# Performance work log

Hardware: AMD Instinct MI355X
Metric: run time of the kernel (lower is better)

Reference implementation:

```python
import jax, jax.numpy as jnp
from jax import lax
import numpy as np

T, B, NI, D = 512, 128, 512, 512  # time, batch, input dim, hidden dim


def setup_inputs() -> dict:
    key = jax.random.key(0)
    k1, k2, k3, k4 = jax.random.split(key, 4)
    stdv = 1.0 / np.sqrt(D)
    return {
        "X": jax.random.normal(k1, (T, B, NI), dtype=jnp.float32),
        "Wf": jax.random.uniform(k2, (NI, 4 * D), jnp.float32, -stdv, stdv),
        "Wr": jax.random.uniform(k3, (D, 4 * D), jnp.float32, -stdv, stdv),
        "bf": jax.random.uniform(k4, (4 * D,), jnp.float32, -2 * stdv, 2 * stdv),
        "i": jnp.ones((T, B), dtype=jnp.float32),
        "h0": jnp.zeros((B, D), dtype=jnp.float32),
        "c0": jnp.zeros((B, D), dtype=jnp.float32),
    }


def reference(X, Wf, Wr, bf, i, h0, c0):
    # Precompute input contribution to all gates: [T, B, 4D]
    intern = jnp.einsum('tbi,ig->tbg', X, Wf) + bf

    def step(carry, inp):
        h, c = carry           # h: [B,D] (previous masked output), c: [B,D]
        z, m = inp             # z: [B,4D], m: [B] validity mask
        z = z + h @ Wr
        cin = jnp.tanh(z[:, :D])                 # cell input
        ig = jax.nn.sigmoid(z[:, D:2 * D])       # input gate
        fg = jax.nn.sigmoid(z[:, 2 * D:3 * D])   # forget gate
        og = jax.nn.sigmoid(z[:, 3 * D:])        # output gate
        m = m[:, None]
        c_new = m * (c * fg + cin * ig) + (1.0 - m) * c
        y = m * (og * jnp.tanh(c_new))           # output zeroed on invalid frames
        return (y, c_new), (y, c_new)

    (_, d), (Y, C) = lax.scan(step, (h0, c0), (intern, i))
    # Matches module: returns (Y, (C, d)) -> flattened here
    return Y, C, d
```

## Files before the change

kernel.cpp:

```cpp
#include <hip/hip_runtime.h>
#include <hip/hip_bf16.h>
#include <hip/hip_fp16.h>

#define T_STEPS 512
#define BATCH   128
#define NID     512
#define DH      512
#define KTOT    1024
#define NG      2048

using f16x8 = __attribute__((ext_vector_type(8))) _Float16;
using f32x4 = __attribute__((ext_vector_type(4))) float;

__device__ __forceinline__ float sigmoid_fast(float x) {
    return 1.0f / (1.0f + __expf(-x));
}
__device__ __forceinline__ float tanh_fast(float x) {
    float ax = fabsf(x);
    float e = __expf(2.0f * ax);
    float r = 1.0f - 2.0f / (e + 1.0f);
    return copysignf(r, x);
}

__global__ void prep_weights(const float* __restrict__ Wf,
                             const float* __restrict__ Wr,
                             const float* __restrict__ bf,
                             _Float16* __restrict__ WT,
                             float* __restrict__ bfa) {
    int orow = blockIdx.x;
    int d = orow >> 2;
    int g = orow & 3;
    int col = g * DH + d;
    for (int e = 0; e < 4; ++e) {
        int k = (e << 8) + threadIdx.x;
        float v = (k < NID) ? Wf[(size_t)k * NG + col]
                            : Wr[(size_t)(k - NID) * NG + col];
        WT[(size_t)orow * KTOT + k] = (_Float16)v;
    }
    if (threadIdx.x == 0) bfa[orow] = bf[col];
}

__global__ void prep_state(const float* __restrict__ h0,
                           const float* __restrict__ c0,
                           _Float16* __restrict__ h,
                           float* __restrict__ c) {
    int base = blockIdx.x * 1024 + threadIdx.x;
    for (int e = 0; e < 4; ++e) {
        int i = base + e * 256;
        h[i] = (_Float16)h0[i];
        c[i] = c0[i];
    }
}

__global__ __launch_bounds__(256)
void lstm_step(const float* __restrict__ X,
               const float* __restrict__ imask,
               const _Float16* __restrict__ WT,
               const float* __restrict__ bfa,
               const _Float16* __restrict__ hin,
               _Float16* __restrict__ hout,
               float* __restrict__ c,
               float* __restrict__ Yout,
               float* __restrict__ Cout,
               float* __restrict__ dout,
               int t) {
    __shared__ float zs[32][68];

    const int tid  = threadIdx.x;
    const int lane = tid & 63;
    const int w    = tid >> 6;
    const int l15  = lane & 15;
    const int l4   = lane >> 4;

    const int b0  = blockIdx.x * 32;
    const int gc0 = blockIdx.y * 64;

    const int rt  = w & 1;
    const int ct0 = (w >> 1) * 2;

    const int arow = b0 + rt * 16 + l15;
    const float*    xrow = X + ((size_t)t * BATCH + arow) * NID;
    const _Float16* hrow = hin + (size_t)arow * DH;

    const int koff = l4 * 8;

    const _Float16* bp0 = WT + (size_t)(gc0 + 16 * ct0 + l15) * KTOT + koff;
    const _Float16* bp1 = WT + (size_t)(gc0 + 16 * (ct0 + 1) + l15) * KTOT + koff;

    f32x4 acc0 = {0.f, 0.f, 0.f, 0.f};
    f32x4 acc1 = {0.f, 0.f, 0.f, 0.f};

    #pragma unroll 4
    for (int k0 = 0; k0 < KTOT; k0 += 32) {
        f16x8 a;
        if (k0 < NID) {
            const float* xp = xrow + k0 + koff;
            f32x4 v0 = *(const f32x4*)xp;
            f32x4 v1 = *(const f32x4*)(xp + 4);
            a[0] = (_Float16)v0[0]; a[1] = (_Float16)v0[1];
            a[2] = (_Float16)v0[2]; a[3] = (_Float16)v0[3];
            a[4] = (_Float16)v1[0]; a[5] = (_Float16)v1[1];
            a[6] = (_Float16)v1[2]; a[7] = (_Float16)v1[3];
        } else {
            a = *(const f16x8*)(hrow + (k0 - NID) + koff);
        }
        f16x8 bf0 = *(const f16x8*)(bp0 + k0);
        f16x8 bf1 = *(const f16x8*)(bp1 + k0);
        acc0 = __builtin_amdgcn_mfma_f32_16x16x32_f16(a, bf0, acc0, 0, 0, 0);
        acc1 = __builtin_amdgcn_mfma_f32_16x16x32_f16(a, bf1, acc1, 0, 0, 0);
    }

    #pragma unroll
    for (int rg = 0; rg < 4; ++rg) {
        int row = rt * 16 + l4 * 4 + rg;
        zs[row][16 * ct0 + l15]       = acc0[rg];
        zs[row][16 * (ct0 + 1) + l15] = acc1[rg];
    }
    __syncthreads();

    #pragma unroll
    for (int q = 0; q < 2; ++q) {
        int idx = q * 256 + tid;
        int r  = idx >> 4;
        int dl = idx & 15;
        int b     = b0 + r;
        int dglob = blockIdx.y * 16 + dl;

        f32x4 bb = *(const f32x4*)(bfa + gc0 + dl * 4);
        float z0 = zs[r][dl * 4 + 0] + bb[0];
        float z1 = zs[r][dl * 4 + 1] + bb[1];
        float z2 = zs[r][dl * 4 + 2] + bb[2];
        float z3 = zs[r][dl * 4 + 3] + bb[3];

        float cin = tanh_fast(z0);
        float ig  = sigmoid_fast(z1);
        float fg  = sigmoid_fast(z2);
        float og  = sigmoid_fast(z3);

        float m    = imask[(size_t)t * BATCH + b];
        float cold = c[b * DH + dglob];
        float cnew = m * (cold * fg + cin * ig) + (1.0f - m) * cold;
        float y    = m * (og * tanh_fast(cnew));

        size_t oidx = ((size_t)t * BATCH + b) * DH + dglob;
        Yout[oidx] = y;
        Cout[oidx] = cnew;
        c[b * DH + dglob]    = cnew;
        hout[b * DH + dglob] = (_Float16)y;
        if (t == T_STEPS - 1) dout[b * DH + dglob] = cnew;
    }
}

extern "C" void kernel_launch(void* const* d_in, const int* in_sizes, int n_in,
                              void* d_out, int out_size, void* d_ws, size_t ws_size,
                              hipStream_t stream) {
    const float* X  = (const float*)d_in[0];
    const float* Wf = (const float*)d_in[1];
    const float* Wr = (const float*)d_in[2];
    const float* bf = (const float*)d_in[3];
    const float* im = (const float*)d_in[4];
    const float* h0 = (const float*)d_in[5];
    const float* c0 = (const float*)d_in[6];

    char* ws = (char*)d_ws;
    _Float16* WT   = (_Float16*)ws;
    float*    bfa  = (float*)(ws + (4u << 20));
    _Float16* hb0  = (_Float16*)(ws + (4u << 20) + 8192);
    _Float16* hb1  = hb0 + BATCH * DH;
    float*    cbuf = (float*)(hb1 + BATCH * DH);

    float* Yout = (float*)d_out;
    float* Cout = Yout + (size_t)T_STEPS * BATCH * DH;
    float* dout = Cout + (size_t)T_STEPS * BATCH * DH;

    hipLaunchKernelGGL(prep_weights, dim3(2048), dim3(256), 0, stream, Wf, Wr, bf, WT, bfa);
    hipLaunchKernelGGL(prep_state,   dim3(64),   dim3(256), 0, stream, h0, c0, hb0, cbuf);

    for (int t = 0; t < T_STEPS; ++t) {
        const _Float16* hin = (t & 1) ? hb1 : hb0;
        _Float16*      hout = (t & 1) ? hb0 : hb1;
        hipLaunchKernelGGL(lstm_step, dim3(4, 32), dim3(256), 0, stream,
                           X, im, WT, bfa, hin, hout, cbuf, Yout, Cout, dout, t);
    }
}
```

Baseline: 11.46 ms.

## Replace per-step launches with a persistent cooperative kernel using grid sync

```diff
diff --git a/kernel.cpp b/kernel.cpp
--- a/kernel.cpp
+++ b/kernel.cpp
@@ -1,6 +1,8 @@
 #include <hip/hip_runtime.h>
-#include <hip/hip_bf16.h>
 #include <hip/hip_fp16.h>
+#include <hip/hip_cooperative_groups.h>
+
+namespace cg = cooperative_groups;
 
 #define T_STEPS 512
 #define BATCH   128
@@ -8,42 +10,174 @@
 #define DH      512
 #define KTOT    1024
 #define NG      2048
+#define TC      64
+#define NCHUNK  (T_STEPS / TC)
+#define NWG     256
+#define NTHR    256
 
 using f16x8 = __attribute__((ext_vector_type(8))) _Float16;
 using f32x4 = __attribute__((ext_vector_type(4))) float;
 
-__device__ __forceinline__ float sigmoid_fast(float x) {
-    return 1.0f / (1.0f + __expf(-x));
-}
+__device__ __forceinline__ float sigmoid_fast(float x) { return 1.0f / (1.0f + __expf(-x)); }
 __device__ __forceinline__ float tanh_fast(float x) {
     float ax = fabsf(x);
-    float e = __expf(2.0f * ax);
-    float r = 1.0f - 2.0f / (e + 1.0f);
+    float e  = __expf(2.0f * ax);
+    float r  = 1.0f - 2.0f / (e + 1.0f);
     return copysignf(r, x);
 }
 
-__global__ void prep_weights(const float* __restrict__ Wf,
-                             const float* __restrict__ Wr,
-                             const float* __restrict__ bf,
-                             _Float16* __restrict__ WT,
+__global__ __launch_bounds__(NTHR, 1)
+void lstm_persist(const float* __restrict__ X,
+                  const float* __restrict__ Wf,
+                  const float* __restrict__ Wr,
+                  const float* __restrict__ bfs,
+                  const float* __restrict__ imask,
+                  const float* __restrict__ h0,
+                  const float* __restrict__ c0,
+                  _Float16* __restrict__ WT,
+                  float* __restrict__ bfa,
+                  _Float16* __restrict__ hb,
+                  float* __restrict__ cbuf,
+                  _Float16* __restrict__ zbuf,
+                  float* __restrict__ Yout,
+                  float* __restrict__ Cout,
+                  float* __restrict__ dout)
+{
+    cg::grid_group grid = cg::this_grid();
+    const int tid  = threadIdx.x;
+    const int wg   = blockIdx.x;
+    const int lane = tid & 63;
+    const int wv   = tid >> 6;
+    const int l15  = lane & 15;
+    const int l4   = lane >> 4;
+
+    __shared__ float zs[4][16][17];
+
+    #pragma unroll
+    for (int rr = 0; rr < 8; ++rr) {
+        int orow = wg * 8 + rr;
+        int d = orow >> 2, g = orow & 3;
+        int col = g * DH + d;
+        #pragma unroll
+        for (int e = 0; e < 4; ++e) {
+            int k = e * NTHR + tid;
+            float v = (k < NID) ? Wf[(size_t)k * NG + col]
+                                : Wr[(size_t)(k - NID) * NG + col];
+            WT[(size_t)orow * KTOT + k] = (_Float16)v;
+        }
+    }
+    int gtid = wg * NTHR + tid;
+    if (gtid < NG) { int d = gtid >> 2, g = gtid & 3; bfa[gtid] = bfs[g * DH + d]; }
+    hb[gtid]   = (_Float16)h0[gtid];
+    cbuf[gtid] = c0[gtid];
+    grid.sync();
+
+    const int cgidx = wg & 127;
+    const int rh    = wg >> 7;
+    const int mycol = cgidx * 16 + l15;
+    f16x8 Bres[16];
+    #pragma unroll
+    for (int s = 0; s < 16; ++s)
+        Bres[s] = *(const f16x8*)(WT + (size_t)mycol * KTOT + NID + s * 32 + l4 * 8);
+
+    for (int ck = 0; ck < NCHUNK; ++ck) {
+        for (int it = 0; it < 16; ++it) {
+            int tile = it * NWG + wg;
+            int cb = tile & 31;
+            int rb = tile >> 5;
+            int mrow = rb * 64 + wv * 16 + l15;
+            const float* xrow = X + ((size_t)ck * 8192 + mrow) * NID;
+            f32x4 acc[4] = {{0.f,0.f,0.f,0.f},{0.f,0.f,0.f,0.f},
+                            {0.f,0.f,0.f,0.f},{0.f,0.f,0.f,0.f}};
+            #pragma unroll 4
+            for (int s = 0; s < 16; ++s) {
+                int k = s * 32 + l4 * 8;
+                f32x4 x0 = *(const f32x4*)(xrow + k);
+                f32x4 x1 = *(const f32x4*)(xrow + k + 4);
+                f16x8 a;
+                a[0]=(_Float16)x0[0]; a[1]=(_Float16)x0[1];
+                a[2]=(_Float16)x0[2]; a[3]=(_Float16)x0[3];
+                a[4]=(_Float16)x1[0]; a[5]=(_Float16)x1[1];
+                a[6]=(_Float16)x1[2]; a[7]=(_Float16)x1[3];
+                #pragma unroll
+                for (int ct = 0; ct < 4; ++ct) {
+                    f16x8 b = *(const f16x8*)(WT + (size_t)(cb*64 + ct*16 + l15) * KTOT + k);
+                    acc[ct] = __builtin_amdgcn_mfma_f32_16x16x32_f16(a, b, acc[ct], 0, 0, 0);
+                }
+            }
+            #pragma unroll
+            for (int ct = 0; ct < 4; ++ct) {
+                int col = cb * 64 + ct * 16 + l15;
+                float bias = bfa[col];
+                #pragma unroll
+                for (int j = 0; j < 4; ++j) {
+                    int row = rb * 64 + wv * 16 + l4 * 4 + j;
+                    zbuf[(size_t)row * NG + col] = (_Float16)(acc[ct][j] + bias);
+                }
+            }
+        }
+        grid.sync();
+
+        for (int tc = 0; tc < TC; ++tc) {
+            int t = ck * TC + tc;
+            const _Float16* hin  = hb + (size_t)(t & 1) * (BATCH * DH);
+            _Float16*       hout = hb + (size_t)((t + 1) & 1) * (BATCH * DH);
+
+            int arow = rh * 64 + wv * 16 + l15;
+            f32x4 acc = {0.f, 0.f, 0.f, 0.f};
+            #pragma unroll
+            for (int s = 0; s < 16; ++s) {
+                f16x8 a = *(const f16x8*)(hin + (size_t)arow * DH + s * 32 + l4 * 8);
+                acc = __builtin_amdgcn_mfma_f32_16x16x32_f16(a, Bres[s], acc, 0, 0, 0);
+            }
+            #pragma unroll
+            for (int j = 0; j < 4; ++j) {
+                int brow = rh * 64 + wv * 16 + l4 * 4 + j;
+                float z = (float)zbuf[(size_t)(tc * BATCH + brow) * NG + cgidx * 16 + l15];
+                zs[wv][l4 * 4 + j][l15] = acc[j] + z;
+            }
+            int rr = lane >> 2, dl = lane & 3;
+            int b  = rh * 64 + wv * 16 + rr;
+            int d  = cgidx * 4 + dl;
+            float z0 = zs[wv][rr][dl * 4 + 0];
+            float z1 = zs[wv][rr][dl * 4 + 1];
+            float z2 = zs[wv][rr][dl * 4 + 2];
+            float z3 = zs[wv][rr][dl * 4 + 3];
+            float cin = tanh_fast(z0);
+            float ig  = sigmoid_fast(z1);
+            float fg  = sigmoid_fast(z2);
+            float og  = sigmoid_fast(z3);
+            float mm   = imask[(size_t)t * BATCH + b];
+            float cold = cbuf[b * DH + d];
+            float cnew = mm * (cold * fg + cin * ig) + (1.0f - mm) * cold;
+            float y    = mm * (og * tanh_fast(cnew));
+            cbuf[b * DH + d] = cnew;
+            size_t o = ((size_t)t * BATCH + b) * DH + d;
+            Yout[o] = y;
+            Cout[o] = cnew;
+            hout[b * DH + d] = (_Float16)y;
+            if (t == T_STEPS - 1) dout[b * DH + d] = cnew;
+            grid.sync();
+        }
+    }
+}
+
+__global__ void prep_weights(const float* __restrict__ Wf, const float* __restrict__ Wr,
+                             const float* __restrict__ bf, _Float16* __restrict__ WT,
                              float* __restrict__ bfa) {
     int orow = blockIdx.x;
-    int d = orow >> 2;
-    int g = orow & 3;
+    int d = orow >> 2, g = orow & 3;
     int col = g * DH + d;
     for (int e = 0; e < 4; ++e) {
         int k = (e << 8) + threadIdx.x;
-        float v = (k < NID) ? Wf[(size_t)k * NG + col]
-                            : Wr[(size_t)(k - NID) * NG + col];
+        float v = (k < NID) ? Wf[(size_t)k * NG + col] : Wr[(size_t)(k - NID) * NG + col];
         WT[(size_t)orow * KTOT + k] = (_Float16)v;
     }
     if (threadIdx.x == 0) bfa[orow] = bf[col];
 }
 
-__global__ void prep_state(const float* __restrict__ h0,
-                           const float* __restrict__ c0,
-                           _Float16* __restrict__ h,
-                           float* __restrict__ c) {
+__global__ void prep_state(const float* __restrict__ h0, const float* __restrict__ c0,
+                           _Float16* __restrict__ h, float* __restrict__ c) {
     int base = blockIdx.x * 1024 + threadIdx.x;
     for (int e = 0; e < 4; ++e) {
         int i = base + e * 256;
@@ -53,43 +187,24 @@
 }
 
 __global__ __launch_bounds__(256)
-void lstm_step(const float* __restrict__ X,
-               const float* __restrict__ imask,
-               const _Float16* __restrict__ WT,
-               const float* __restrict__ bfa,
-               const _Float16* __restrict__ hin,
-               _Float16* __restrict__ hout,
-               float* __restrict__ c,
-               float* __restrict__ Yout,
-               float* __restrict__ Cout,
-               float* __restrict__ dout,
-               int t) {
-    __shared__ float zs[32][68];
-
-    const int tid  = threadIdx.x;
-    const int lane = tid & 63;
-    const int w    = tid >> 6;
-    const int l15  = lane & 15;
-    const int l4   = lane >> 4;
-
-    const int b0  = blockIdx.x * 32;
-    const int gc0 = blockIdx.y * 64;
-
-    const int rt  = w & 1;
-    const int ct0 = (w >> 1) * 2;
-
+void lstm_step(const float* __restrict__ X, const float* __restrict__ imask,
+               const _Float16* __restrict__ WT, const float* __restrict__ bfa,
+               const _Float16* __restrict__ hin, _Float16* __restrict__ hout,
+               float* __restrict__ c, float* __restrict__ Yout,
+               float* __restrict__ Cout, float* __restrict__ dout, int t) {
+    __shared__ float zsl[32][68];
+    const int tid = threadIdx.x;
+    const int lane = tid & 63, w = tid >> 6;
+    const int l15 = lane & 15, l4 = lane >> 4;
+    const int b0 = blockIdx.x * 32, gc0 = blockIdx.y * 64;
+    const int rt = w & 1, ct0 = (w >> 1) * 2;
     const int arow = b0 + rt * 16 + l15;
-    const float*    xrow = X + ((size_t)t * BATCH + arow) * NID;
+    const float* xrow = X + ((size_t)t * BATCH + arow) * NID;
     const _Float16* hrow = hin + (size_t)arow * DH;
-
     const int koff = l4 * 8;
-
     const _Float16* bp0 = WT + (size_t)(gc0 + 16 * ct0 + l15) * KTOT + koff;
     const _Float16* bp1 = WT + (size_t)(gc0 + 16 * (ct0 + 1) + l15) * KTOT + koff;
-
-    f32x4 acc0 = {0.f, 0.f, 0.f, 0.f};
-    f32x4 acc1 = {0.f, 0.f, 0.f, 0.f};
-
+    f32x4 acc0 = {0.f,0.f,0.f,0.f}, acc1 = {0.f,0.f,0.f,0.f};
     #pragma unroll 4
     for (int k0 = 0; k0 < KTOT; k0 += 32) {
         f16x8 a;
@@ -97,10 +212,8 @@
             const float* xp = xrow + k0 + koff;
             f32x4 v0 = *(const f32x4*)xp;
             f32x4 v1 = *(const f32x4*)(xp + 4);
-            a[0] = (_Float16)v0[0]; a[1] = (_Float16)v0[1];
-            a[2] = (_Float16)v0[2]; a[3] = (_Float16)v0[3];
-            a[4] = (_Float16)v1[0]; a[5] = (_Float16)v1[1];
-            a[6] = (_Float16)v1[2]; a[7] = (_Float16)v1[3];
+            a[0]=(_Float16)v0[0]; a[1]=(_Float16)v0[1]; a[2]=(_Float16)v0[2]; a[3]=(_Float16)v0[3];
+            a[4]=(_Float16)v1[0]; a[5]=(_Float16)v1[1]; a[6]=(_Float16)v1[2]; a[7]=(_Float16)v1[3];
         } else {
             a = *(const f16x8*)(hrow + (k0 - NID) + koff);
         }
@@ -109,43 +222,32 @@
         acc0 = __builtin_amdgcn_mfma_f32_16x16x32_f16(a, bf0, acc0, 0, 0, 0);
         acc1 = __builtin_amdgcn_mfma_f32_16x16x32_f16(a, bf1, acc1, 0, 0, 0);
     }
-
     #pragma unroll
     for (int rg = 0; rg < 4; ++rg) {
         int row = rt * 16 + l4 * 4 + rg;
-        zs[row][16 * ct0 + l15]       = acc0[rg];
-        zs[row][16 * (ct0 + 1) + l15] = acc1[rg];
+        zsl[row][16 * ct0 + l15]       = acc0[rg];
+        zsl[row][16 * (ct0 + 1) + l15] = acc1[rg];
     }
     __syncthreads();
-
     #pragma unroll
     for (int q = 0; q < 2; ++q) {
         int idx = q * 256 + tid;
-        int r  = idx >> 4;
-        int dl = idx & 15;
-        int b     = b0 + r;
-        int dglob = blockIdx.y * 16 + dl;
-
+        int r = idx >> 4, dl = idx & 15;
+        int b = b0 + r, dglob = blockIdx.y * 16 + dl;
         f32x4 bb = *(const f32x4*)(bfa + gc0 + dl * 4);
-        float z0 = zs[r][dl * 4 + 0] + bb[0];
-        float z1 = zs[r][dl * 4 + 1] + bb[1];
-        float z2 = zs[r][dl * 4 + 2] + bb[2];
-        float z3 = zs[r][dl * 4 + 3] + bb[3];
-
-        float cin = tanh_fast(z0);
-        float ig  = sigmoid_fast(z1);
-        float fg  = sigmoid_fast(z2);
-        float og  = sigmoid_fast(z3);
-
-        float m    = imask[(size_t)t * BATCH + b];
+        float z0 = zsl[r][dl*4+0] + bb[0];
+        float z1 = zsl[r][dl*4+1] + bb[1];
+        float z2 = zsl[r][dl*4+2] + bb[2];
+        float z3 = zsl[r][dl*4+3] + bb[3];
+        float cin = tanh_fast(z0), ig = sigmoid_fast(z1);
+        float fg = sigmoid_fast(z2), og = sigmoid_fast(z3);
+        float m = imask[(size_t)t * BATCH + b];
         float cold = c[b * DH + dglob];
         float cnew = m * (cold * fg + cin * ig) + (1.0f - m) * cold;
-        float y    = m * (og * tanh_fast(cnew));
-
+        float y = m * (og * tanh_fast(cnew));
         size_t oidx = ((size_t)t * BATCH + b) * DH + dglob;
-        Yout[oidx] = y;
-        Cout[oidx] = cnew;
-        c[b * DH + dglob]    = cnew;
+        Yout[oidx] = y; Cout[oidx] = cnew;
+        c[b * DH + dglob] = cnew;
         hout[b * DH + dglob] = (_Float16)y;
         if (t == T_STEPS - 1) dout[b * DH + dglob] = cnew;
     }
@@ -165,17 +267,27 @@
     char* ws = (char*)d_ws;
     _Float16* WT   = (_Float16*)ws;
     float*    bfa  = (float*)(ws + (4u << 20));
-    _Float16* hb0  = (_Float16*)(ws + (4u << 20) + 8192);
-    _Float16* hb1  = hb0 + BATCH * DH;
-    float*    cbuf = (float*)(hb1 + BATCH * DH);
+    _Float16* hb   = (_Float16*)(ws + (4u << 20) + 8192);
+    float*    cbuf = (float*)(ws + (4u << 20) + 8192 + 262144);
+    _Float16* zbuf = (_Float16*)(ws + (8u << 20));
 
     float* Yout = (float*)d_out;
     float* Cout = Yout + (size_t)T_STEPS * BATCH * DH;
     float* dout = Cout + (size_t)T_STEPS * BATCH * DH;
 
+    bool coop_ok = ws_size >= ((8u << 20) + (size_t)TC * BATCH * NG * sizeof(_Float16));
+    if (coop_ok) {
+        void* args[] = {(void*)&X, (void*)&Wf, (void*)&Wr, (void*)&bf, (void*)&im,
+                        (void*)&h0, (void*)&c0, (void*)&WT, (void*)&bfa, (void*)&hb,
+                        (void*)&cbuf, (void*)&zbuf, (void*)&Yout, (void*)&Cout, (void*)&dout};
+        hipError_t e = hipLaunchCooperativeKernel((void*)lstm_persist, dim3(NWG), dim3(NTHR),
+                                                  args, 0, stream);
+        if (e == hipSuccess) return;
+    }
     hipLaunchKernelGGL(prep_weights, dim3(2048), dim3(256), 0, stream, Wf, Wr, bf, WT, bfa);
-    hipLaunchKernelGGL(prep_state,   dim3(64),   dim3(256), 0, stream, h0, c0, hb0, cbuf);
-
+    _Float16* hb0 = hb;
+    _Float16* hb1 = hb + BATCH * DH;
+    hipLaunchKernelGGL(prep_state, dim3(64), dim3(256), 0, stream, h0, c0, hb0, cbuf);
     for (int t = 0; t < T_STEPS; ++t) {
         const _Float16* hin = (t & 1) ? hb1 : hb0;
         _Float16*      hout = (t & 1) ? hb0 : hb1;
```

Result: slower. 19.49 ms (+70.0%).
